# Kernel optimization log

Measured on AMD Instinct MI355X. Metric: run time of the kernel, lower is better.

Reference implementation:

```python
import jax, jax.numpy as jnp
import numpy as np

N = 16384
FPS_RATIO = 0.5
RADIUS = 0.25
MAX_NEIGHBORS = 10
C_IN, C_HID, C_OUT = 3, 64, 128


def setup_inputs() -> dict:
    key = jax.random.key(0)
    k0, k1, k2 = jax.random.split(key, 3)
    pos = jax.random.uniform(k0, (N, 3), dtype=jnp.float32)
    batch = jnp.zeros((N,), dtype=jnp.int32)  # single point cloud
    W1 = jax.random.normal(k1, (C_IN, C_HID), dtype=jnp.float32) / np.float32(np.sqrt(C_IN))
    b1 = jnp.zeros((C_HID,), jnp.float32)
    W2 = jax.random.normal(k2, (C_HID, C_OUT), dtype=jnp.float32) / np.float32(np.sqrt(C_HID))
    b2 = jnp.zeros((C_OUT,), jnp.float32)
    return {"pos": pos, "batch": batch, "W1": W1, "b1": b1, "W2": W2, "b2": b2}


def _fps(pos, n_samples):
    # iterative farthest point sampling, deterministic start at index 0
    n = pos.shape[0]
    init = (jnp.full((n,), jnp.finfo(jnp.float32).max, jnp.float32), jnp.int32(0))
    def step(carry, _):
        min_d, last = carry
        d = jnp.sum((pos - pos[last]) ** 2, axis=-1)
        min_d = jnp.minimum(min_d, d)
        nxt = jnp.argmax(min_d).astype(jnp.int32)
        return (min_d, nxt), last
    _, idx = jax.lax.scan(step, init, None, length=n_samples)
    return idx


def _forward(pos, W1, b1, W2, b2):
    n = pos.shape[0]
    s = int(n * FPS_RATIO)
    idx = jax.lax.stop_gradient(_fps(pos, s))          # [S] sampled centers
    centers = pos[idx]                                  # [S,3]
    # ball query: squared distances from each center to all points  [S,N]
    d2 = jnp.sum((centers[:, None, :] - pos[None, :, :]) ** 2, axis=-1)
    neg_d2, src = jax.lax.top_k(-d2, MAX_NEIGHBORS)     # [S,K] nearest-first
    valid = neg_d2 >= -(RADIUS ** 2)                    # within the ball
    # edge_index = stack([col, row]): source = src (full-set idx),
    # target = row (sampled-set idx in [0,S)). PointNetConv does pos_i = pos[row],
    # i.e. indexes the FULL pos with sampled-set indices -> pos[:s].
    pos_i = pos[:s]                                     # [S,3]
    rel = pos[src] - pos_i[:, None, :]                  # [S,K,3] pos_j - pos_i
    # local_mlp (Linear->ReLU->Linear) on each edge message
    h = jax.nn.relu(rel @ W1 + b1) @ W2 + b2            # [S,K,C_OUT]
    h = jnp.where(valid[..., None], h, jnp.float32(-jnp.inf))
    tgt = jnp.repeat(jnp.arange(s, dtype=jnp.int32), MAX_NEIGHBORS)
    out = jax.ops.segment_max(h.reshape(-1, C_OUT), tgt, num_segments=n)  # [N,C]
    # nodes with no incoming edges -> 0 (PyG scatter-max empty fill)
    return jnp.where(jnp.isfinite(out), out, jnp.float32(0.0))


def reference(pos, batch, W1, b1, W2, b2):
    return _forward(pos, W1, b1, W2, b2)
```

## Files before the change

### kernel.cpp

```cpp
#include <hip/hip_runtime.h>

typedef unsigned int u32;
typedef unsigned long long u64;
typedef float f32x2 __attribute__((ext_vector_type(2)));

#define N_PTS 16384
#define N_S   8192
#define NB    10
#define CHID  64
#define COUT  128
#define R2    0.0625f
#define NCELL 4096

__global__ void zero_hist(int* __restrict__ hist) {
  hist[blockIdx.x * 256 + threadIdx.x] = 0;
}

__device__ __forceinline__ u32 spread3(u32 v) {
  return (v & 1u) | ((v & 2u) << 2) | ((v & 4u) << 4) | ((v & 8u) << 6);
}

__global__ void cell_kernel(const float* __restrict__ pos, int* __restrict__ cellid,
                            int* __restrict__ hist) {
  int i = blockIdx.x * 256 + threadIdx.x;
  float x = pos[3 * i], y = pos[3 * i + 1], z = pos[3 * i + 2];
  u32 ix = (u32)(x * 16.0f); if (ix > 15u) ix = 15u;
  u32 iy = (u32)(y * 16.0f); if (iy > 15u) iy = 15u;
  u32 iz = (u32)(z * 16.0f); if (iz > 15u) iz = 15u;
  u32 c = spread3(ix) | (spread3(iy) << 1) | (spread3(iz) << 2);
  cellid[i] = (int)c;
  atomicAdd(&hist[c], 1);
}

__global__ __launch_bounds__(1024) void scan_kernel(const int* __restrict__ hist,
                                                    int* __restrict__ base) {
  __shared__ int sp[1024];
  int t = threadIdx.x;
  int h0 = hist[4 * t], h1 = hist[4 * t + 1], h2 = hist[4 * t + 2], h3 = hist[4 * t + 3];
  int s = h0 + h1 + h2 + h3;
  int acc = s;
  sp[t] = s;
  __syncthreads();
  for (int off = 1; off < 1024; off <<= 1) {
    int v = (t >= off) ? sp[t - off] : 0;
    __syncthreads();
    acc += v;
    sp[t] = acc;
    __syncthreads();
  }
  int excl = acc - s;
  base[4 * t + 0] = excl;
  base[4 * t + 1] = excl + h0;
  base[4 * t + 2] = excl + h0 + h1;
  base[4 * t + 3] = excl + h0 + h1 + h2;
}

__global__ void scatter_kernel(const float* __restrict__ pos, const int* __restrict__ cellid,
                               int* __restrict__ base, float* __restrict__ xs,
                               float* __restrict__ ys, float* __restrict__ zs,
                               int* __restrict__ oid) {
  int i = blockIdx.x * 256 + threadIdx.x;
  int c = cellid[i];
  int d = atomicAdd(&base[c], 1);
  xs[d] = pos[3 * i]; ys[d] = pos[3 * i + 1]; zs[d] = pos[3 * i + 2];
  oid[d] = i;
}

#define FPS_T 1024
#define PPT   16

#define PT_LIST(OP) OP(0) OP(1) OP(2) OP(3) OP(4) OP(5) OP(6) OP(7) \
                    OP(8) OP(9) OP(10) OP(11) OP(12) OP(13) OP(14) OP(15)
#define G4_LIST(OP) OP(0,0,1,2,3,0,1)   OP(1,4,5,6,7,2,3) \
                    OP(2,8,9,10,11,4,5) OP(3,12,13,14,15,6,7)
#define PR_LIST(OP) OP(0) OP(1) OP(2) OP(3) OP(4) OP(5) OP(6) OP(7)

__device__ __forceinline__ u64 u64fmax(u64 a, u64 b) {
  double ad = __longlong_as_double((long long)a);
  double bd = __longlong_as_double((long long)b);
  return (u64)(long long)__double_as_longlong(fmax(ad, bd));
}

template <int CTRL, int RM>
__device__ __forceinline__ u64 dppmax(u64 cur) {
  int slo = __builtin_amdgcn_update_dpp(0, (int)(u32)cur, CTRL, RM, 0xf, false);
  int shi = __builtin_amdgcn_update_dpp(0, (int)(u32)(cur >> 32), CTRL, RM, 0xf, false);
  u64 o = ((u64)(u32)shi << 32) | (u32)slo;
  return u64fmax(o, cur);
}

__device__ __forceinline__ f32x2 pk_add(f32x2 a, f32x2 b) {
  f32x2 d;
  asm("v_pk_add_f32 %0, %1, %2" : "=v"(d) : "v"(a), "v"(b));
  return d;
}
__device__ __forceinline__ f32x2 pk_mul(f32x2 a, f32x2 b) {
  f32x2 d;
  asm("v_pk_mul_f32 %0, %1, %2" : "=v"(d) : "v"(a), "v"(b));
  return d;
}

__global__ __launch_bounds__(FPS_T, 4)
void fps_kernel(const float* __restrict__ pos,
                const float* __restrict__ xs,
                const float* __restrict__ ys,
                const float* __restrict__ zs,
                const int* __restrict__ oidv,
                int* __restrict__ idx_out) {
  __shared__ float2 s_yz[PPT * FPS_T];
  __shared__ u64 s_k[2][16];
  const int t = threadIdx.x;
  const int wv = t >> 6;
  const int base0 = t * PPT;
  const float4* __restrict__ xv = (const float4*)(xs + base0);
  const float4* __restrict__ yv = (const float4*)(ys + base0);
  const float4* __restrict__ zv = (const float4*)(zs + base0);
  const int4*   __restrict__ ov = (const int4*)(oidv + base0);

#define DECLP(J) float md##J;
  PT_LIST(DECLP)
#undef DECLP
#define DECLC(J) u32 C##J;
  PT_LIST(DECLC)
#undef DECLC
#define DECLX(P) f32x2 X##P; f32x2 Y##P; f32x2 Z##P;
  PR_LIST(DECLX)
#undef DECLX

  float bnx = 3.4e38f, bxx = -3.4e38f, bny = 3.4e38f, bxy = -3.4e38f,
        bnz = 3.4e38f, bxz = -3.4e38f;

#define INIT4(G, J0, J1, J2, J3, PA, PB) { \
    float4 vx = xv[G], vy = yv[G], vz = zv[G]; int4 vo = ov[G]; \
    md##J0 = 3.402823466e38f; md##J1 = 3.402823466e38f; \
    md##J2 = 3.402823466e38f; md##J3 = 3.402823466e38f; \
    X##PA.x = vx.x; X##PA.y = vx.y; X##PB.x = vx.z; X##PB.y = vx.w; \
    Y##PA.x = vy.x; Y##PA.y = vy.y; Y##PB.x = vy.z; Y##PB.y = vy.w; \
    Z##PA.x = vz.x; Z##PA.y = vz.y; Z##PB.x = vz.z; Z##PB.y = vz.w; \
    s_yz[J0 * FPS_T + t] = make_float2(vy.x, vz.x); \
    s_yz[J1 * FPS_T + t] = make_float2(vy.y, vz.y); \
    s_yz[J2 * FPS_T + t] = make_float2(vy.z, vz.z); \
    s_yz[J3 * FPS_T + t] = make_float2(vy.w, vz.w); \
    C##J0 = ((16383u - (u32)vo.x) << 14) | (u32)(base0 + J0); \
    C##J1 = ((16383u - (u32)vo.y) << 14) | (u32)(base0 + J1); \
    C##J2 = ((16383u - (u32)vo.z) << 14) | (u32)(base0 + J2); \
    C##J3 = ((16383u - (u32)vo.w) << 14) | (u32)(base0 + J3); \
    bnx = fminf(bnx, fminf(fminf(vx.x, vx.y), fminf(vx.z, vx.w))); \
    bxx = fmaxf(bxx, fmaxf(fmaxf(vx.x, vx.y), fmaxf(vx.z, vx.w))); \
    bny = fminf(bny, fminf(fminf(vy.x, vy.y), fminf(vy.z, vy.w))); \
    bxy = fmaxf(bxy, fmaxf(fmaxf(vy.x, vy.y), fmaxf(vy.z, vy.w))); \
    bnz = fminf(bnz, fminf(fminf(vz.x, vz.y), fminf(vz.z, vz.w))); \
    bxz = fmaxf(bxz, fmaxf(fmaxf(vz.x, vz.y), fmaxf(vz.z, vz.w))); }
  G4_LIST(INIT4)
#undef INIT4

  u64 ckey = 0;
  u64 wklast = 0;
  float cmaxf = 3.402823466e38f;
  float cx = pos[0], cy = pos[1], cz = pos[2];
  if (t == 0) idx_out[0] = 0;
  __syncthreads();

  for (int k = 0; k < N_S - 1; ++k) {
    float dxl = fmaxf(fmaxf(bnx - cx, cx - bxx), 0.0f);
    float dyl = fmaxf(fmaxf(bny - cy, cy - bxy), 0.0f);
    float dzl = fmaxf(fmaxf(bnz - cz, cz - bxz), 0.0f);
    float lb2 = dxl * dxl + dyl * dyl + dzl * dzl;
    bool act = (0.99f * lb2 < cmaxf);

    if (__ballot(act)) {
      if (act) {
        f32x2 ncx2; ncx2.x = -cx; ncx2.y = -cx;
        f32x2 ncy2; ncy2.x = -cy; ncy2.y = -cy;
        f32x2 ncz2; ncz2.x = -cz; ncz2.y = -cz;
        u64 bkA = 0, bkB = 0;
#define UPDP(P, J0, J1) { \
        f32x2 dx2 = pk_add(X##P, ncx2); \
        f32x2 dy2 = pk_add(Y##P, ncy2); \
        f32x2 dz2 = pk_add(Z##P, ncz2); \
        f32x2 sq = pk_add(pk_mul(dx2, dx2), pk_mul(dy2, dy2)); \
        f32x2 d2 = pk_add(sq, pk_mul(dz2, dz2)); \
        float m0 = fminf(md##J0, d2.x); md##J0 = m0; \
        bkA = u64fmax(bkA, ((u64)__float_as_uint(m0) << 32) | C##J0); \
        float m1 = fminf(md##J1, d2.y); md##J1 = m1; \
        bkB = u64fmax(bkB, ((u64)__float_as_uint(m1) << 32) | C##J1); }
        UPDP(0, 0, 1)  UPDP(1, 2, 3)  UPDP(2, 4, 5)  UPDP(3, 6, 7)
        UPDP(4, 8, 9)  UPDP(5, 10, 11) UPDP(6, 12, 13) UPDP(7, 14, 15)
#undef UPDP
        ckey = u64fmax(bkA, bkB);
        cmaxf = __uint_as_float((u32)(ckey >> 32));
      }
      u64 wk = ckey;
      wk = dppmax<0x111, 0xf>(wk);
      wk = dppmax<0x112, 0xf>(wk);
      wk = dppmax<0x114, 0xf>(wk);
      wk = dppmax<0x118, 0xf>(wk);
      wk = dppmax<0x142, 0xa>(wk);
      wk = dppmax<0x143, 0xc>(wk);
      wklast = wk;
    }
    if ((t & 63) == 63) s_k[k & 1][wv] = wklast;
    __syncthreads();

    u64 gk = s_k[k & 1][t & 15];
    gk = dppmax<0x121, 0xf>(gk);
    gk = dppmax<0x122, 0xf>(gk);
    gk = dppmax<0x124, 0xf>(gk);
    gk = dppmax<0x128, 0xf>(gk);
    u32 glo = (u32)__builtin_amdgcn_readfirstlane((int)(u32)gk);
    u32 ghi = (u32)__builtin_amdgcn_readfirstlane((int)(u32)(gk >> 32));
    u64 gmax = ((u64)ghi << 32) | glo;
    int sidx = (int)(gmax & 16383u);
    if (t == 0) idx_out[k + 1] = 16383 - (int)((gmax >> 14) & 16383u);
    int cell = (sidx & (PPT - 1)) * FPS_T + (sidx >> 4);
    cx = xs[sidx];
    float2 yz = s_yz[cell];
    cy = yz.x;
    cz = yz.y;
  }
}

__global__ void zero_tail(float4* __restrict__ outv, int count) {
  int i = blockIdx.x * blockDim.x + threadIdx.x;
  if (i < count) outv[i] = make_float4(0.f, 0.f, 0.f, 0.f);
}

#define KNN_T  1024
#define KNS    32
#define KTILE  1024
#define KPAD   321

__global__ __launch_bounds__(KNN_T) void knn_kernel(const float* __restrict__ pos,
                                                    const int* __restrict__ fps_idx,
                                                    int* __restrict__ src_out,
                                                    int* __restrict__ valid_out) {
  __shared__ float4 s_p[KTILE];
  __shared__ float spd[32][KPAD];
  __shared__ int   spi[32][KPAD];
  const int t = threadIdx.x;
  const int sp = t >> 5;
  const int cl = t & 31;
  const int i = blockIdx.x * 32 + cl;
  const int ci = fps_idx[i];
  const float cx = pos[3 * ci], cy = pos[3 * ci + 1], cz = pos[3 * ci + 2];
  float nd[NB]; int ni[NB];
#pragma unroll
  for (int q = 0; q < NB; ++q) { nd[q] = 3.402823466e38f; ni[q] = 0x7fffffff; }

  for (int base = 0; base < N_PTS; base += KTILE) {
    __syncthreads();
    for (int j = t; j < KTILE; j += KNN_T) {
      int pnt = base + j;
      s_p[j] = make_float4(pos[3 * pnt], pos[3 * pnt + 1], pos[3 * pnt + 2], 0.f);
    }
    __syncthreads();
    for (int j = sp; j < KTILE; j += KNS) {
      float4 q4 = s_p[j];
      float dx = __fsub_rn(cx, q4.x);
      float dy = __fsub_rn(cy, q4.y);
      float dz = __fsub_rn(cz, q4.z);
      float d2 = __fadd_rn(__fadd_rn(__fmul_rn(dx, dx), __fmul_rn(dy, dy)), __fmul_rn(dz, dz));
      if (d2 < nd[NB - 1]) {
        float cd = d2; int cp = base + j;
#pragma unroll
        for (int q = 0; q < NB; ++q) {
          bool sw = (cd < nd[q]) || (cd == nd[q] && cp < ni[q]);
          if (sw) { float td = nd[q]; int tp = ni[q]; nd[q] = cd; ni[q] = cp; cd = td; cp = tp; }
        }
      }
    }
  }
#pragma unroll
  for (int q = 0; q < NB; ++q) { spd[cl][sp * NB + q] = nd[q]; spi[cl][sp * NB + q] = ni[q]; }
  __syncthreads();
  if (sp == 0) {
    int cur[KNS];
#pragma unroll
    for (int s = 0; s < KNS; ++s) cur[s] = 0;
    int vb = 0;
    for (int q = 0; q < NB; ++q) {
      float bd = 3.402823466e38f; int bi = 0x7fffffff; int bsl = 0;
#pragma unroll
      for (int s = 0; s < KNS; ++s) {
        float d = spd[cl][s * NB + cur[s]]; int id = spi[cl][s * NB + cur[s]];
        if (d < bd || (d == bd && id < bi)) { bd = d; bi = id; bsl = s; }
      }
#pragma unroll
      for (int s = 0; s < KNS; ++s) cur[s] += (s == bsl) ? 1 : 0;
      src_out[i * NB + q] = bi;
      if (bd <= R2) vb |= (1 << q);
    }
    valid_out[i] = vb;
  }
}

#define MLP_T 128
#define W2S   68

__global__ __launch_bounds__(MLP_T) void mlp_kernel(const float* __restrict__ pos,
                                                    const int* __restrict__ src,
                                                    const int* __restrict__ valid,
                                                    const float* __restrict__ W1,
                                                    const float* __restrict__ b1,
                                                    const float* __restrict__ W2,
                                                    const float* __restrict__ b2,
                                                    float* __restrict__ out) {
  __shared__ float sW2T[COUT * W2S];
  __shared__ float sW1[3 * CHID];
  __shared__ float sb1[CHID];
  __shared__ float sh1[NB][CHID];
  __shared__ float srel[NB][3];
  __shared__ int   svalid;
  const int t = threadIdx.x;
  const int i = blockIdx.x;

  for (int kk = 0; kk < CHID; ++kk) sW2T[t * W2S + kk] = W2[kk * COUT + t];
  for (int e = t; e < 3 * CHID; e += MLP_T) sW1[e] = W1[e];
  if (t < CHID) sb1[t] = b1[t];
  if (t < NB) {
    int s = src[i * NB + t];
    srel[t][0] = pos[3 * s + 0] - pos[3 * i + 0];
    srel[t][1] = pos[3 * s + 1] - pos[3 * i + 1];
    srel[t][2] = pos[3 * s + 2] - pos[3 * i + 2];
  }
  if (t == 0) svalid = valid[i];
  __syncthreads();

  for (int e = t; e < NB * CHID; e += MLP_T) {
    int n = e >> 6, kk = e & 63;
    float a = sb1[kk] + srel[n][0] * sW1[kk] + srel[n][1] * sW1[64 + kk] + srel[n][2] * sW1[128 + kk];
    sh1[n][kk] = fmaxf(a, 0.0f);
  }
  __syncthreads();

  const int vmask = svalid;
  const float bb = b2[t];
  float m = 0.0f;
  bool any = false;
  for (int n = 0; n < NB; ++n) {
    if (vmask & (1 << n)) {
      float acc = bb;
#pragma unroll
      for (int kk = 0; kk < CHID; kk += 4) {
        float4 w = *(const float4*)&sW2T[t * W2S + kk];
        float4 h = *(const float4*)&sh1[n][kk];
        acc = fmaf(h.x, w.x, acc);
        acc = fmaf(h.y, w.y, acc);
        acc = fmaf(h.z, w.z, acc);
        acc = fmaf(h.w, w.w, acc);
      }
      m = any ? fmaxf(m, acc) : acc;
      any = true;
    }
  }
  out[i * COUT + t] = any ? m : 0.0f;
}

extern "C" void kernel_launch(void* const* d_in, const int* in_sizes, int n_in,
                              void* d_out, int out_size, void* d_ws, size_t ws_size,
                              hipStream_t stream) {
  (void)in_sizes; (void)n_in; (void)out_size; (void)ws_size;
  const float* pos = (const float*)d_in[0];
  const float* W1 = (const float*)d_in[2];
  const float* b1 = (const float*)d_in[3];
  const float* W2 = (const float*)d_in[4];
  const float* b2 = (const float*)d_in[5];
  float* out = (float*)d_out;

  char* ws = (char*)d_ws;
  int*   idx   = (int*)ws;                 ws += (size_t)N_S * 4;
  int*   src   = (int*)ws;                 ws += (size_t)N_S * NB * 4;
  int*   valid = (int*)ws;                 ws += (size_t)N_S * 4;
  float* xs    = (float*)ws;               ws += (size_t)N_PTS * 4;
  float* ys    = (float*)ws;               ws += (size_t)N_PTS * 4;
  float* zs    = (float*)ws;               ws += (size_t)N_PTS * 4;
  int*   oid   = (int*)ws;                 ws += (size_t)N_PTS * 4;
  int* cellid = src;
  int* hist   = src + N_PTS;
  int* basebuf= src + N_PTS + NCELL;

  zero_hist<<<NCELL / 256, 256, 0, stream>>>(hist);
  cell_kernel<<<N_PTS / 256, 256, 0, stream>>>(pos, cellid, hist);
  scan_kernel<<<1, 1024, 0, stream>>>(hist, basebuf);
  scatter_kernel<<<N_PTS / 256, 256, 0, stream>>>(pos, cellid, basebuf, xs, ys, zs, oid);
  fps_kernel<<<1, FPS_T, 0, stream>>>(pos, xs, ys, zs, oid, idx);
  {
    int count = (N_PTS - N_S) * COUT / 4;
    zero_tail<<<(count + 255) / 256, 256, 0, stream>>>((float4*)(out + (size_t)N_S * COUT), count);
  }
  knn_kernel<<<N_S / 32, KNN_T, 0, stream>>>(pos, idx, src, valid);
  mlp_kernel<<<N_S, MLP_T, 0, stream>>>(pos, src, valid, W1, b1, W2, b2, out);
}
```

Measured before the change: 7.243 ms.

## Fuse FPS, kNN and MLP into one persistent kernel with progress-flag overlap

```diff
diff --git a/kernel.cpp b/kernel.cpp
--- a/kernel.cpp
+++ b/kernel.cpp
@@ -11,10 +11,6 @@
 #define COUT  128
 #define R2    0.0625f
 #define NCELL 4096
-
-__global__ void zero_hist(int* __restrict__ hist) {
-  hist[blockIdx.x * 256 + threadIdx.x] = 0;
-}
 
 __device__ __forceinline__ u32 spread3(u32 v) {
   return (v & 1u) | ((v & 2u) << 2) | ((v & 4u) << 4) | ((v & 8u) << 6);
@@ -68,6 +64,22 @@
 
 #define FPS_T 1024
 #define PPT   16
+#define WRK   192
+#define NCHK  (N_S / 32)
+
+#define OFF_SK   131072
+#define OFF_SPD  16384
+#define OFF_SPI  57472
+#define OFF_W2T  98560
+#define OFF_W1   133376
+#define OFF_B1   134144
+#define OFF_PROG 134400
+#define SMEM_SZ  134432
+
+#define KNS    32
+#define KTILE  1024
+#define KPAD   321
+#define W2S    68
 
 #define PT_LIST(OP) OP(0) OP(1) OP(2) OP(3) OP(4) OP(5) OP(6) OP(7) \
                     OP(8) OP(9) OP(10) OP(11) OP(12) OP(13) OP(14) OP(15)
@@ -100,35 +112,46 @@
   return d;
 }
 
-__global__ __launch_bounds__(FPS_T, 4)
-void fps_kernel(const float* __restrict__ pos,
-                const float* __restrict__ xs,
-                const float* __restrict__ ys,
-                const float* __restrict__ zs,
-                const int* __restrict__ oidv,
-                int* __restrict__ idx_out) {
-  __shared__ float2 s_yz[PPT * FPS_T];
-  __shared__ u64 s_k[2][16];
+__global__ __launch_bounds__(1024, 4)
+void fused_kernel(const float* __restrict__ pos,
+                  const float* __restrict__ xs,
+                  const float* __restrict__ ys,
+                  const float* __restrict__ zs,
+                  const int* __restrict__ oidv,
+                  int* __restrict__ idx,
+                  int* __restrict__ src,
+                  int* __restrict__ valid,
+                  const float* __restrict__ W1,
+                  const float* __restrict__ b1,
+                  const float* __restrict__ W2,
+                  const float* __restrict__ b2,
+                  float* __restrict__ out,
+                  int* __restrict__ prog) {
+  __shared__ __align__(16) unsigned char smem[SMEM_SZ];
   const int t = threadIdx.x;
-  const int wv = t >> 6;
-  const int base0 = t * PPT;
-  const float4* __restrict__ xv = (const float4*)(xs + base0);
-  const float4* __restrict__ yv = (const float4*)(ys + base0);
-  const float4* __restrict__ zv = (const float4*)(zs + base0);
-  const int4*   __restrict__ ov = (const int4*)(oidv + base0);
+
+  if (blockIdx.x == 0) {
+    float2* s_yz = (float2*)smem;
+    u64 (*s_k)[16] = (u64 (*)[16])(smem + OFF_SK);
+    const int wv = t >> 6;
+    const int base0 = t * PPT;
+    const float4* __restrict__ xv = (const float4*)(xs + base0);
+    const float4* __restrict__ yv = (const float4*)(ys + base0);
+    const float4* __restrict__ zv = (const float4*)(zs + base0);
+    const int4*   __restrict__ ov = (const int4*)(oidv + base0);
 
 #define DECLP(J) float md##J;
-  PT_LIST(DECLP)
+    PT_LIST(DECLP)
 #undef DECLP
 #define DECLC(J) u32 C##J;
-  PT_LIST(DECLC)
+    PT_LIST(DECLC)
 #undef DECLC
 #define DECLX(P) f32x2 X##P; f32x2 Y##P; f32x2 Z##P;
-  PR_LIST(DECLX)
+    PR_LIST(DECLX)
 #undef DECLX
 
-  float bnx = 3.4e38f, bxx = -3.4e38f, bny = 3.4e38f, bxy = -3.4e38f,
-        bnz = 3.4e38f, bxz = -3.4e38f;
+    float bnx = 3.4e38f, bxx = -3.4e38f, bny = 3.4e38f, bxy = -3.4e38f,
+          bnz = 3.4e38f, bxz = -3.4e38f;
 
 #define INIT4(G, J0, J1, J2, J3, PA, PB) { \
     float4 vx = xv[G], vy = yv[G], vz = zv[G]; int4 vo = ov[G]; \
@@ -151,209 +174,216 @@
     bxy = fmaxf(bxy, fmaxf(fmaxf(vy.x, vy.y), fmaxf(vy.z, vy.w))); \
     bnz = fminf(bnz, fminf(fminf(vz.x, vz.y), fminf(vz.z, vz.w))); \
     bxz = fmaxf(bxz, fmaxf(fmaxf(vz.x, vz.y), fmaxf(vz.z, vz.w))); }
-  G4_LIST(INIT4)
+    G4_LIST(INIT4)
 #undef INIT4
 
-  u64 ckey = 0;
-  u64 wklast = 0;
-  float cmaxf = 3.402823466e38f;
-  float cx = pos[0], cy = pos[1], cz = pos[2];
-  if (t == 0) idx_out[0] = 0;
-  __syncthreads();
-
-  for (int k = 0; k < N_S - 1; ++k) {
-    float dxl = fmaxf(fmaxf(bnx - cx, cx - bxx), 0.0f);
-    float dyl = fmaxf(fmaxf(bny - cy, cy - bxy), 0.0f);
-    float dzl = fmaxf(fmaxf(bnz - cz, cz - bxz), 0.0f);
-    float lb2 = dxl * dxl + dyl * dyl + dzl * dzl;
-    bool act = (0.99f * lb2 < cmaxf);
-
-    if (__ballot(act)) {
-      if (act) {
-        f32x2 ncx2; ncx2.x = -cx; ncx2.y = -cx;
-        f32x2 ncy2; ncy2.x = -cy; ncy2.y = -cy;
-        f32x2 ncz2; ncz2.x = -cz; ncz2.y = -cz;
-        u64 bkA = 0, bkB = 0;
+    u64 ckey = 0;
+    u64 wklast = 0;
+    float cmaxf = 3.402823466e38f;
+    float cx = pos[0], cy = pos[1], cz = pos[2];
+    if (t == 0) idx[0] = 0;
+    __syncthreads();
+
+    for (int k = 0; k < N_S - 1; ++k) {
+      float dxl = fmaxf(fmaxf(bnx - cx, cx - bxx), 0.0f);
+      float dyl = fmaxf(fmaxf(bny - cy, cy - bxy), 0.0f);
+      float dzl = fmaxf(fmaxf(bnz - cz, cz - bxz), 0.0f);
+      float lb2 = dxl * dxl + dyl * dyl + dzl * dzl;
+      bool act = (0.99f * lb2 < cmaxf);
+
+      if (__ballot(act)) {
+        if (act) {
+          f32x2 ncx2; ncx2.x = -cx; ncx2.y = -cx;
+          f32x2 ncy2; ncy2.x = -cy; ncy2.y = -cy;
+          f32x2 ncz2; ncz2.x = -cz; ncz2.y = -cz;
+          u64 bkA = 0, bkB = 0;
 #define UPDP(P, J0, J1) { \
-        f32x2 dx2 = pk_add(X##P, ncx2); \
-        f32x2 dy2 = pk_add(Y##P, ncy2); \
-        f32x2 dz2 = pk_add(Z##P, ncz2); \
-        f32x2 sq = pk_add(pk_mul(dx2, dx2), pk_mul(dy2, dy2)); \
-        f32x2 d2 = pk_add(sq, pk_mul(dz2, dz2)); \
-        float m0 = fminf(md##J0, d2.x); md##J0 = m0; \
-        bkA = u64fmax(bkA, ((u64)__float_as_uint(m0) << 32) | C##J0); \
-        float m1 = fminf(md##J1, d2.y); md##J1 = m1; \
-        bkB = u64fmax(bkB, ((u64)__float_as_uint(m1) << 32) | C##J1); }
-        UPDP(0, 0, 1)  UPDP(1, 2, 3)  UPDP(2, 4, 5)  UPDP(3, 6, 7)
-        UPDP(4, 8, 9)  UPDP(5, 10, 11) UPDP(6, 12, 13) UPDP(7, 14, 15)
+          f32x2 dx2 = pk_add(X##P, ncx2); \
+          f32x2 dy2 = pk_add(Y##P, ncy2); \
+          f32x2 dz2 = pk_add(Z##P, ncz2); \
+          f32x2 sq = pk_add(pk_mul(dx2, dx2), pk_mul(dy2, dy2)); \
+          f32x2 d2 = pk_add(sq, pk_mul(dz2, dz2)); \
+          float m0 = fminf(md##J0, d2.x); md##J0 = m0; \
+          bkA = u64fmax(bkA, ((u64)__float_as_uint(m0) << 32) | C##J0); \
+          float m1 = fminf(md##J1, d2.y); md##J1 = m1; \
+          bkB = u64fmax(bkB, ((u64)__float_as_uint(m1) << 32) | C##J1); }
+          UPDP(0, 0, 1)  UPDP(1, 2, 3)  UPDP(2, 4, 5)  UPDP(3, 6, 7)
+          UPDP(4, 8, 9)  UPDP(5, 10, 11) UPDP(6, 12, 13) UPDP(7, 14, 15)
 #undef UPDP
-        ckey = u64fmax(bkA, bkB);
-        cmaxf = __uint_as_float((u32)(ckey >> 32));
-      }
-      u64 wk = ckey;
-      wk = dppmax<0x111, 0xf>(wk);
-      wk = dppmax<0x112, 0xf>(wk);
-      wk = dppmax<0x114, 0xf>(wk);
-      wk = dppmax<0x118, 0xf>(wk);
-      wk = dppmax<0x142, 0xa>(wk);
-      wk = dppmax<0x143, 0xc>(wk);
-      wklast = wk;
+          ckey = u64fmax(bkA, bkB);
+          cmaxf = __uint_as_float((u32)(ckey >> 32));
+        }
+        u64 wk = ckey;
+        wk = dppmax<0x111, 0xf>(wk);
+        wk = dppmax<0x112, 0xf>(wk);
+        wk = dppmax<0x114, 0xf>(wk);
+        wk = dppmax<0x118, 0xf>(wk);
+        wk = dppmax<0x142, 0xa>(wk);
+        wk = dppmax<0x143, 0xc>(wk);
+        wklast = wk;
+      }
+      if ((t & 63) == 63) s_k[k & 1][wv] = wklast;
+      __syncthreads();
+
+      u64 gk = s_k[k & 1][t & 15];
+      gk = dppmax<0x121, 0xf>(gk);
+      gk = dppmax<0x122, 0xf>(gk);
+      gk = dppmax<0x124, 0xf>(gk);
+      gk = dppmax<0x128, 0xf>(gk);
+      u32 glo = (u32)__builtin_amdgcn_readfirstlane((int)(u32)gk);
+      u32 ghi = (u32)__builtin_amdgcn_readfirstlane((int)(u32)(gk >> 32));
+      u64 gmax = ((u64)ghi << 32) | glo;
+      int sidx = (int)(gmax & 16383u);
+      if (t == 0) {
+        idx[k + 1] = 16383 - (int)((gmax >> 14) & 16383u);
+        if ((k & 31) == 30)
+          __hip_atomic_store(prog, k + 2, __ATOMIC_RELEASE, __HIP_MEMORY_SCOPE_AGENT);
+      }
+      int cell = (sidx & (PPT - 1)) * FPS_T + (sidx >> 4);
+      cx = xs[sidx];
+      float2 yz = s_yz[cell];
+      cy = yz.x;
+      cz = yz.y;
     }
-    if ((t & 63) == 63) s_k[k & 1][wv] = wklast;
-    __syncthreads();
-
-    u64 gk = s_k[k & 1][t & 15];
-    gk = dppmax<0x121, 0xf>(gk);
-    gk = dppmax<0x122, 0xf>(gk);
-    gk = dppmax<0x124, 0xf>(gk);
-    gk = dppmax<0x128, 0xf>(gk);
-    u32 glo = (u32)__builtin_amdgcn_readfirstlane((int)(u32)gk);
-    u32 ghi = (u32)__builtin_amdgcn_readfirstlane((int)(u32)(gk >> 32));
-    u64 gmax = ((u64)ghi << 32) | glo;
-    int sidx = (int)(gmax & 16383u);
-    if (t == 0) idx_out[k + 1] = 16383 - (int)((gmax >> 14) & 16383u);
-    int cell = (sidx & (PPT - 1)) * FPS_T + (sidx >> 4);
-    cx = xs[sidx];
-    float2 yz = s_yz[cell];
-    cy = yz.x;
-    cz = yz.y;
-  }
-}
-
-__global__ void zero_tail(float4* __restrict__ outv, int count) {
-  int i = blockIdx.x * blockDim.x + threadIdx.x;
-  if (i < count) outv[i] = make_float4(0.f, 0.f, 0.f, 0.f);
-}
-
-#define KNN_T  1024
-#define KNS    32
-#define KTILE  1024
-#define KPAD   321
-
-__global__ __launch_bounds__(KNN_T) void knn_kernel(const float* __restrict__ pos,
-                                                    const int* __restrict__ fps_idx,
-                                                    int* __restrict__ src_out,
-                                                    int* __restrict__ valid_out) {
-  __shared__ float4 s_p[KTILE];
-  __shared__ float spd[32][KPAD];
-  __shared__ int   spi[32][KPAD];
-  const int t = threadIdx.x;
-  const int sp = t >> 5;
-  const int cl = t & 31;
-  const int i = blockIdx.x * 32 + cl;
-  const int ci = fps_idx[i];
-  const float cx = pos[3 * ci], cy = pos[3 * ci + 1], cz = pos[3 * ci + 2];
-  float nd[NB]; int ni[NB];
-#pragma unroll
-  for (int q = 0; q < NB; ++q) { nd[q] = 3.402823466e38f; ni[q] = 0x7fffffff; }
-
-  for (int base = 0; base < N_PTS; base += KTILE) {
-    __syncthreads();
-    for (int j = t; j < KTILE; j += KNN_T) {
-      int pnt = base + j;
-      s_p[j] = make_float4(pos[3 * pnt], pos[3 * pnt + 1], pos[3 * pnt + 2], 0.f);
+  } else {
+    const int wid = blockIdx.x - 1;
+    float4* s_p = (float4*)smem;
+    float (*spd)[KPAD] = (float (*)[KPAD])(smem + OFF_SPD);
+    int   (*spi)[KPAD] = (int (*)[KPAD])(smem + OFF_SPI);
+    float* sW2T = (float*)(smem + OFF_W2T);
+    float* sW1  = (float*)(smem + OFF_W1);
+    float* sb1  = (float*)(smem + OFF_B1);
+    int*   sprog = (int*)(smem + OFF_PROG);
+    float* msh1  = (float*)(smem + OFF_SPD);
+    float* msrel = (float*)(smem + OFF_SPI);
+
+    for (int e = t; e < CHID * COUT; e += 1024) {
+      int kk = e >> 7, c = e & (COUT - 1);
+      sW2T[c * W2S + kk] = W2[e];
+    }
+    if (t < 3 * CHID) sW1[t] = W1[t];
+    if (t < CHID) sb1[t] = b1[t];
+    {
+      float4* outv = (float4*)(out + (size_t)N_S * COUT);
+      const int cnt = (N_PTS - N_S) * COUT / 4;
+      for (int j = wid * 1024 + t; j < cnt; j += WRK * 1024)
+        outv[j] = make_float4(0.f, 0.f, 0.f, 0.f);
     }
     __syncthreads();
-    for (int j = sp; j < KTILE; j += KNS) {
-      float4 q4 = s_p[j];
-      float dx = __fsub_rn(cx, q4.x);
-      float dy = __fsub_rn(cy, q4.y);
-      float dz = __fsub_rn(cz, q4.z);
-      float d2 = __fadd_rn(__fadd_rn(__fmul_rn(dx, dx), __fmul_rn(dy, dy)), __fmul_rn(dz, dz));
-      if (d2 < nd[NB - 1]) {
-        float cd = d2; int cp = base + j;
-#pragma unroll
+
+    for (int gc = wid; gc < NCHK; gc += WRK) {
+      const int need = gc * 32 + 32;
+      for (;;) {
+        if (t == 0) *sprog = __hip_atomic_load(prog, __ATOMIC_ACQUIRE, __HIP_MEMORY_SCOPE_AGENT);
+        __syncthreads();
+        if (*sprog >= need) break;
+        __builtin_amdgcn_s_sleep(32);
+        __syncthreads();
+      }
+      const int sp = t >> 5;
+      const int cl = t & 31;
+      const int i = gc * 32 + cl;
+      const int ci = __hip_atomic_load(idx + i, __ATOMIC_RELAXED, __HIP_MEMORY_SCOPE_AGENT);
+      const float cx = pos[3 * ci], cy = pos[3 * ci + 1], cz = pos[3 * ci + 2];
+      float nd[NB]; int ni[NB];
+#pragma unroll
+      for (int q = 0; q < NB; ++q) { nd[q] = 3.402823466e38f; ni[q] = 0x7fffffff; }
+
+      for (int base = 0; base < N_PTS; base += KTILE) {
+        __syncthreads();
+        for (int j = t; j < KTILE; j += 1024) {
+          int pnt = base + j;
+          s_p[j] = make_float4(pos[3 * pnt], pos[3 * pnt + 1], pos[3 * pnt + 2], 0.f);
+        }
+        __syncthreads();
+        for (int j = sp; j < KTILE; j += KNS) {
+          float4 q4 = s_p[j];
+          float dx = __fsub_rn(cx, q4.x);
+          float dy = __fsub_rn(cy, q4.y);
+          float dz = __fsub_rn(cz, q4.z);
+          float d2 = __fadd_rn(__fadd_rn(__fmul_rn(dx, dx), __fmul_rn(dy, dy)), __fmul_rn(dz, dz));
+          if (d2 < nd[NB - 1]) {
+            float cd = d2; int cp = base + j;
+#pragma unroll
+            for (int q = 0; q < NB; ++q) {
+              bool sw = (cd < nd[q]) || (cd == nd[q] && cp < ni[q]);
+              if (sw) { float td = nd[q]; int tp = ni[q]; nd[q] = cd; ni[q] = cp; cd = td; cp = tp; }
+            }
+          }
+        }
+      }
+#pragma unroll
+      for (int q = 0; q < NB; ++q) { spd[cl][sp * NB + q] = nd[q]; spi[cl][sp * NB + q] = ni[q]; }
+      __syncthreads();
+      if (sp == 0) {
+        int cur[KNS];
+#pragma unroll
+        for (int s = 0; s < KNS; ++s) cur[s] = 0;
+        int vb = 0;
         for (int q = 0; q < NB; ++q) {
-          bool sw = (cd < nd[q]) || (cd == nd[q] && cp < ni[q]);
-          if (sw) { float td = nd[q]; int tp = ni[q]; nd[q] = cd; ni[q] = cp; cd = td; cp = tp; }
-        }
+          float bd = 3.402823466e38f; int bi = 0x7fffffff; int bsl = 0;
+#pragma unroll
+          for (int s = 0; s < KNS; ++s) {
+            float d = spd[cl][s * NB + cur[s]]; int id = spi[cl][s * NB + cur[s]];
+            if (d < bd || (d == bd && id < bi)) { bd = d; bi = id; bsl = s; }
+          }
+#pragma unroll
+          for (int s = 0; s < KNS; ++s) cur[s] += (s == bsl) ? 1 : 0;
+          src[i * NB + q] = bi;
+          if (bd <= R2) vb |= (1 << q);
+        }
+        valid[i] = vb;
+      }
+      __syncthreads();
+
+      for (int r = 0; r < 4; ++r) {
+        const int c8 = t >> 7;
+        const int ch = t & 127;
+        const int im = gc * 32 + r * 8 + c8;
+        if (ch < NB) {
+          int s = src[im * NB + ch];
+          msrel[(c8 * NB + ch) * 3 + 0] = pos[3 * s + 0] - pos[3 * im + 0];
+          msrel[(c8 * NB + ch) * 3 + 1] = pos[3 * s + 1] - pos[3 * im + 1];
+          msrel[(c8 * NB + ch) * 3 + 2] = pos[3 * s + 2] - pos[3 * im + 2];
+        }
+        __syncthreads();
+        for (int e = t; e < 8 * NB * CHID; e += 1024) {
+          int kk = e & 63;
+          int n = (e >> 6) % NB;
+          int cc = e / (NB * CHID);
+          float a = sb1[kk] + msrel[(cc * NB + n) * 3 + 0] * sW1[kk]
+                            + msrel[(cc * NB + n) * 3 + 1] * sW1[64 + kk]
+                            + msrel[(cc * NB + n) * 3 + 2] * sW1[128 + kk];
+          msh1[(cc * NB + n) * CHID + kk] = fmaxf(a, 0.0f);
+        }
+        __syncthreads();
+        {
+          const int vmask = valid[im];
+          const float bb = b2[ch];
+          float m = 0.0f;
+          bool any = false;
+          for (int n = 0; n < NB; ++n) {
+            if (vmask & (1 << n)) {
+              float acc = bb;
+#pragma unroll
+              for (int g = 0; g < 16; ++g) {
+                float4 h = *(const float4*)&msh1[(c8 * NB + n) * CHID + 4 * g];
+                float4 w = *(const float4*)&sW2T[ch * W2S + 4 * g];
+                acc = fmaf(h.x, w.x, acc);
+                acc = fmaf(h.y, w.y, acc);
+                acc = fmaf(h.z, w.z, acc);
+                acc = fmaf(h.w, w.w, acc);
+              }
+              m = any ? fmaxf(m, acc) : acc;
+              any = true;
+            }
+          }
+          out[(size_t)im * COUT + ch] = any ? m : 0.0f;
+        }
+        __syncthreads();
       }
     }
   }
-#pragma unroll
-  for (int q = 0; q < NB; ++q) { spd[cl][sp * NB + q] = nd[q]; spi[cl][sp * NB + q] = ni[q]; }
-  __syncthreads();
-  if (sp == 0) {
-    int cur[KNS];
-#pragma unroll
-    for (int s = 0; s < KNS; ++s) cur[s] = 0;
-    int vb = 0;
-    for (int q = 0; q < NB; ++q) {
-      float bd = 3.402823466e38f; int bi = 0x7fffffff; int bsl = 0;
-#pragma unroll
-      for (int s = 0; s < KNS; ++s) {
-        float d = spd[cl][s * NB + cur[s]]; int id = spi[cl][s * NB + cur[s]];
-        if (d < bd || (d == bd && id < bi)) { bd = d; bi = id; bsl = s; }
-      }
-#pragma unroll
-      for (int s = 0; s < KNS; ++s) cur[s] += (s == bsl) ? 1 : 0;
-      src_out[i * NB + q] = bi;
-      if (bd <= R2) vb |= (1 << q);
-    }
-    valid_out[i] = vb;
-  }
-}
-
-#define MLP_T 128
-#define W2S   68
-
-__global__ __launch_bounds__(MLP_T) void mlp_kernel(const float* __restrict__ pos,
-                                                    const int* __restrict__ src,
-                                                    const int* __restrict__ valid,
-                                                    const float* __restrict__ W1,
-                                                    const float* __restrict__ b1,
-                                                    const float* __restrict__ W2,
-                                                    const float* __restrict__ b2,
-                                                    float* __restrict__ out) {
-  __shared__ float sW2T[COUT * W2S];
-  __shared__ float sW1[3 * CHID];
-  __shared__ float sb1[CHID];
-  __shared__ float sh1[NB][CHID];
-  __shared__ float srel[NB][3];
-  __shared__ int   svalid;
-  const int t = threadIdx.x;
-  const int i = blockIdx.x;
-
-  for (int kk = 0; kk < CHID; ++kk) sW2T[t * W2S + kk] = W2[kk * COUT + t];
-  for (int e = t; e < 3 * CHID; e += MLP_T) sW1[e] = W1[e];
-  if (t < CHID) sb1[t] = b1[t];
-  if (t < NB) {
-    int s = src[i * NB + t];
-    srel[t][0] = pos[3 * s + 0] - pos[3 * i + 0];
-    srel[t][1] = pos[3 * s + 1] - pos[3 * i + 1];
-    srel[t][2] = pos[3 * s + 2] - pos[3 * i + 2];
-  }
-  if (t == 0) svalid = valid[i];
-  __syncthreads();
-
-  for (int e = t; e < NB * CHID; e += MLP_T) {
-    int n = e >> 6, kk = e & 63;
-    float a = sb1[kk] + srel[n][0] * sW1[kk] + srel[n][1] * sW1[64 + kk] + srel[n][2] * sW1[128 + kk];
-    sh1[n][kk] = fmaxf(a, 0.0f);
-  }
-  __syncthreads();
-
-  const int vmask = svalid;
-  const float bb = b2[t];
-  float m = 0.0f;
-  bool any = false;
-  for (int n = 0; n < NB; ++n) {
-    if (vmask & (1 << n)) {
-      float acc = bb;
-#pragma unroll
-      for (int kk = 0; kk < CHID; kk += 4) {
-        float4 w = *(const float4*)&sW2T[t * W2S + kk];
-        float4 h = *(const float4*)&sh1[n][kk];
-        acc = fmaf(h.x, w.x, acc);
-        acc = fmaf(h.y, w.y, acc);
-        acc = fmaf(h.z, w.z, acc);
-        acc = fmaf(h.w, w.w, acc);
-      }
-      m = any ? fmaxf(m, acc) : acc;
-      any = true;
-    }
-  }
-  out[i * COUT + t] = any ? m : 0.0f;
 }
 
 extern "C" void kernel_launch(void* const* d_in, const int* in_sizes, int n_in,
@@ -375,19 +405,16 @@
   float* ys    = (float*)ws;               ws += (size_t)N_PTS * 4;
   float* zs    = (float*)ws;               ws += (size_t)N_PTS * 4;
   int*   oid   = (int*)ws;                 ws += (size_t)N_PTS * 4;
+  int*   progp = (int*)ws;                 ws += 16;
   int* cellid = src;
   int* hist   = src + N_PTS;
   int* basebuf= src + N_PTS + NCELL;
 
-  zero_hist<<<NCELL / 256, 256, 0, stream>>>(hist);
+  hipMemsetAsync(hist, 0, (size_t)NCELL * 4, stream);
+  hipMemsetAsync(progp, 0, 4, stream);
   cell_kernel<<<N_PTS / 256, 256, 0, stream>>>(pos, cellid, hist);
   scan_kernel<<<1, 1024, 0, stream>>>(hist, basebuf);
   scatter_kernel<<<N_PTS / 256, 256, 0, stream>>>(pos, cellid, basebuf, xs, ys, zs, oid);
-  fps_kernel<<<1, FPS_T, 0, stream>>>(pos, xs, ys, zs, oid, idx);
-  {
-    int count = (N_PTS - N_S) * COUT / 4;
-    zero_tail<<<(count + 255) / 256, 256, 0, stream>>>((float4*)(out + (size_t)N_S * COUT), count);
-  }
-  knn_kernel<<<N_S / 32, KNN_T, 0, stream>>>(pos, idx, src, valid);
-  mlp_kernel<<<N_S, MLP_T, 0, stream>>>(pos, src, valid, W1, b1, W2, b2, out);
-}
+  fused_kernel<<<1 + WRK, 1024, 0, stream>>>(pos, xs, ys, zs, oid, idx, src, valid,
+                                             W1, b1, W2, b2, out, progp);
+}
```

Result: slower. 8.980 ms (+24.0%).
